# Kernel optimization log

Hardware: AMD Instinct MI355X
Metric: run time of the kernel (lower is better)

Reference implementation:

```python
import jax, jax.numpy as jnp
import numpy as np

N_CLASSES = 18

def setup_inputs() -> dict:
    key = jax.random.key(0)
    k1, k2 = jax.random.split(key)
    B = 2_000_000
    output = jax.random.normal(k1, (B, N_CLASSES), dtype=jnp.float32)
    labels_soft = jax.random.uniform(k2, (B, N_CLASSES), dtype=jnp.float32)
    return {"output": output, "labels_soft": labels_soft}

def reference(output, labels_soft):
    # Original: sum over classes of mean_b( CE(output, cls) * labels_soft[:, cls] )
    # = mean over batch of sum_c( -log_softmax(output)[b, c] * labels_soft[b, c] )
    logp = jax.nn.log_softmax(output, axis=-1)          # [B, C]
    per_row = -jnp.sum(logp * labels_soft, axis=-1)     # [B]
    return jnp.mean(per_row)
```

## Files before the change

kernel.cpp:

```cpp
#include <hip/hip_runtime.h>

#define NCLS   18
#define TROWS  256
#define TWORDS (TROWS * NCLS)
#define NCHUNK ((TWORDS * 4) / 1024)

#define AS1 __attribute__((address_space(1)))
#define AS3 __attribute__((address_space(3)))

__global__ __launch_bounds__(256) void ce_soft_kernel(
    const float* __restrict__ logits,
    const float* __restrict__ labels,
    float* __restrict__ result,
    int B, float invB)
{
    __shared__ float sX[TWORDS];
    __shared__ float sLse[TROWS];

    const int tid  = threadIdx.x;
    const int lane = tid & 63;
    const int wid  = tid >> 6;

    const int nTiles = B / TROWS;
    float acc = 0.0f;

    for (int tile = blockIdx.x; tile < nTiles; tile += gridDim.x) {
        const float* gx = logits + (size_t)tile * TWORDS;

        for (int c = wid; c < NCHUNK; c += 4) {
            __builtin_amdgcn_global_load_lds(
                (const AS1 void*)(gx + c * 256 + lane * 4),
                (AS3 void*)(sX + c * 256),
                16, 0, 0);
        }
        __syncthreads();

        {
            const float2* r2 = (const float2*)(sX + tid * NCLS);
            float x[NCLS];
            #pragma unroll
            for (int k = 0; k < NCLS / 2; ++k) {
                float2 v = r2[k];
                x[2 * k] = v.x; x[2 * k + 1] = v.y;
            }
            float m = x[0];
            #pragma unroll
            for (int c = 1; c < NCLS; ++c) m = fmaxf(m, x[c]);
            float se = 0.0f;
            #pragma unroll
            for (int c = 0; c < NCLS; ++c) se += __expf(x[c] - m);
            sLse[tid] = m + __logf(se);
        }
        __syncthreads();

        const float2* gl2 = (const float2*)(labels + (size_t)tile * TWORDS);
        const float2* sx2 = (const float2*)sX;
        #pragma unroll
        for (int it = 0; it < TWORDS / 512; ++it) {
            int j = it * 256 + tid;
            float2 lv = gl2[j];
            float2 xv = sx2[j];
            float lse = sLse[j / 9];
            acc = fmaf(lv.x, lse - xv.x, acc);
            acc = fmaf(lv.y, lse - xv.y, acc);
        }
        __syncthreads();
    }

    for (int row = nTiles * TROWS + blockIdx.x * blockDim.x + tid; row < B;
         row += gridDim.x * blockDim.x) {
        const float2* o2 = (const float2*)(logits + (size_t)row * NCLS);
        const float2* l2 = (const float2*)(labels + (size_t)row * NCLS);
        float x[NCLS], l[NCLS];
        #pragma unroll
        for (int k = 0; k < NCLS / 2; ++k) {
            float2 v = o2[k]; x[2 * k] = v.x; x[2 * k + 1] = v.y;
            float2 w = l2[k]; l[2 * k] = w.x; l[2 * k + 1] = w.y;
        }
        float m = x[0];
        #pragma unroll
        for (int c = 1; c < NCLS; ++c) m = fmaxf(m, x[c]);
        float se = 0.0f, dot = 0.0f, sl = 0.0f;
        #pragma unroll
        for (int c = 0; c < NCLS; ++c) {
            se += __expf(x[c] - m);
            dot = fmaf(l[c], x[c], dot);
            sl += l[c];
        }
        float lse = m + __logf(se);
        acc = fmaf(sl, lse, acc - dot);
    }

    #pragma unroll
    for (int off = 32; off > 0; off >>= 1)
        acc += __shfl_down(acc, off, 64);

    __shared__ float wave_sums[4];
    if (lane == 0) wave_sums[wid] = acc;
    __syncthreads();
    if (tid == 0) {
        float s = wave_sums[0] + wave_sums[1] + wave_sums[2] + wave_sums[3];
        atomicAdd(result, s * invB);
    }
}

extern "C" void kernel_launch(void* const* d_in, const int* in_sizes, int n_in,
                              void* d_out, int out_size, void* d_ws, size_t ws_size,
                              hipStream_t stream) {
    const float* logits = (const float*)d_in[0];
    const float* labels = (const float*)d_in[1];
    float* result = (float*)d_out;

    int B = in_sizes[0] / NCLS;

    hipMemsetAsync(d_out, 0, sizeof(float), stream);

    int block = 256;
    int grid  = 2048;
    ce_soft_kernel<<<grid, block, 0, stream>>>(logits, labels, result, B, 1.0f / (float)B);
}
```

Measured before the change: 294.9 us.

## Double-buffer logits and labels into LDS and split each row across two threads

Logits and labels tiles now both stream into LDS through async global-to-LDS loads, into double buffers, so the next tile is fetched while the current one is computed. Each row is handled by a pair of threads that combine max and sum-exp with lane shuffles. The tile shrinks to 128 rows and the grid to 1024 blocks. The atomic accumulation and memset are replaced by per-block partials plus a single-block finish kernel. This adds a second launch and relies on the workspace size, and the prefetch loop issues no explicit wait on the async loads before the barrier.

```diff
diff --git a/kernel.cpp b/kernel.cpp
--- a/kernel.cpp
+++ b/kernel.cpp
@@ -1,74 +1,93 @@
 #include <hip/hip_runtime.h>
 
 #define NCLS   18
-#define TROWS  256
+#define TROWS  128
 #define TWORDS (TROWS * NCLS)
-#define NCHUNK ((TWORDS * 4) / 1024)
+#define CHUNKS (TWORDS / 256)
 
 #define AS1 __attribute__((address_space(1)))
 #define AS3 __attribute__((address_space(3)))
 
-__global__ __launch_bounds__(256) void ce_soft_kernel(
+__global__ __launch_bounds__(256) void ce_soft_main(
     const float* __restrict__ logits,
     const float* __restrict__ labels,
-    float* __restrict__ result,
-    int B, float invB)
+    float* __restrict__ partial,
+    int B)
 {
-    __shared__ float sX[TWORDS];
-    __shared__ float sLse[TROWS];
+    __shared__ float sX[2][TWORDS];
+    __shared__ float sL[2][TWORDS];
+    __shared__ float sWS[4];
 
     const int tid  = threadIdx.x;
     const int lane = tid & 63;
     const int wid  = tid >> 6;
+    const int p    = tid >> 1;
+    const int h    = tid & 1;
+    const int nTiles = B / TROWS;
+    const int grid = gridDim.x;
 
-    const int nTiles = B / TROWS;
     float acc = 0.0f;
+    int cur = 0;
 
-    for (int tile = blockIdx.x; tile < nTiles; tile += gridDim.x) {
-        const float* gx = logits + (size_t)tile * TWORDS;
+    int t0 = blockIdx.x;
+    if (t0 < nTiles) {
+        const float* gx = logits + (size_t)t0 * TWORDS;
+        const float* gl = labels + (size_t)t0 * TWORDS;
+        for (int c = wid; c < CHUNKS; c += 4) {
+            __builtin_amdgcn_global_load_lds((const AS1 void*)(gx + c * 256 + lane * 4),
+                                             (AS3 void*)(&sX[0][c * 256]), 16, 0, 0);
+            __builtin_amdgcn_global_load_lds((const AS1 void*)(gl + c * 256 + lane * 4),
+                                             (AS3 void*)(&sL[0][c * 256]), 16, 0, 0);
+        }
+    }
 
-        for (int c = wid; c < NCHUNK; c += 4) {
-            __builtin_amdgcn_global_load_lds(
-                (const AS1 void*)(gx + c * 256 + lane * 4),
-                (AS3 void*)(sX + c * 256),
-                16, 0, 0);
-        }
+    for (int t = t0; t < nTiles; t += grid) {
         __syncthreads();
 
-        {
-            const float2* r2 = (const float2*)(sX + tid * NCLS);
-            float x[NCLS];
-            #pragma unroll
-            for (int k = 0; k < NCLS / 2; ++k) {
-                float2 v = r2[k];
-                x[2 * k] = v.x; x[2 * k + 1] = v.y;
+        int tn = t + grid;
+        if (tn < nTiles) {
+            const float* gx = logits + (size_t)tn * TWORDS;
+            const float* gl = labels + (size_t)tn * TWORDS;
+            float* dX = &sX[cur ^ 1][0];
+            float* dL = &sL[cur ^ 1][0];
+            for (int c = wid; c < CHUNKS; c += 4) {
+                __builtin_amdgcn_global_load_lds((const AS1 void*)(gx + c * 256 + lane * 4),
+                                                 (AS3 void*)(dX + c * 256), 16, 0, 0);
+                __builtin_amdgcn_global_load_lds((const AS1 void*)(gl + c * 256 + lane * 4),
+                                                 (AS3 void*)(dL + c * 256), 16, 0, 0);
             }
-            float m = x[0];
-            #pragma unroll
-            for (int c = 1; c < NCLS; ++c) m = fmaxf(m, x[c]);
-            float se = 0.0f;
-            #pragma unroll
-            for (int c = 0; c < NCLS; ++c) se += __expf(x[c] - m);
-            sLse[tid] = m + __logf(se);
         }
-        __syncthreads();
 
-        const float2* gl2 = (const float2*)(labels + (size_t)tile * TWORDS);
-        const float2* sx2 = (const float2*)sX;
+        const float2* rx = (const float2*)(&sX[cur][p * NCLS]);
+        const float2* rl = (const float2*)(&sL[cur][p * NCLS]);
+        float2 xv[5], lv[5];
+        const int n = 5 - h;
         #pragma unroll
-        for (int it = 0; it < TWORDS / 512; ++it) {
-            int j = it * 256 + tid;
-            float2 lv = gl2[j];
-            float2 xv = sx2[j];
-            float lse = sLse[j / 9];
-            acc = fmaf(lv.x, lse - xv.x, acc);
-            acc = fmaf(lv.y, lse - xv.y, acc);
+        for (int k = 0; k < 5; ++k) {
+            int c = 2 * k + h;
+            if (k < n) { xv[k] = rx[c];                      lv[k] = rl[c]; }
+            else       { xv[k] = make_float2(-1e30f, -1e30f); lv[k] = make_float2(0.f, 0.f); }
         }
-        __syncthreads();
+        float m = xv[0].x;
+        #pragma unroll
+        for (int k = 0; k < 5; ++k) { m = fmaxf(m, xv[k].x); m = fmaxf(m, xv[k].y); }
+        m = fmaxf(m, __shfl_xor(m, 1, 64));
+        float se = 0.f, dot = 0.f, sl = 0.f;
+        #pragma unroll
+        for (int k = 0; k < 5; ++k) {
+            se += __expf(xv[k].x - m) + __expf(xv[k].y - m);
+            dot = fmaf(lv[k].x, xv[k].x, dot);
+            dot = fmaf(lv[k].y, xv[k].y, dot);
+            sl += lv[k].x + lv[k].y;
+        }
+        se += __shfl_xor(se, 1, 64);
+        float lse = m + __logf(se);
+        acc = fmaf(sl, lse, acc - dot);
+        cur ^= 1;
     }
 
     for (int row = nTiles * TROWS + blockIdx.x * blockDim.x + tid; row < B;
-         row += gridDim.x * blockDim.x) {
+         row += grid * blockDim.x) {
         const float2* o2 = (const float2*)(logits + (size_t)row * NCLS);
         const float2* l2 = (const float2*)(labels + (size_t)row * NCLS);
         float x[NCLS], l[NCLS];
@@ -77,31 +96,43 @@
             float2 v = o2[k]; x[2 * k] = v.x; x[2 * k + 1] = v.y;
             float2 w = l2[k]; l[2 * k] = w.x; l[2 * k + 1] = w.y;
         }
-        float m = x[0];
+        float mm = x[0];
         #pragma unroll
-        for (int c = 1; c < NCLS; ++c) m = fmaxf(m, x[c]);
-        float se = 0.0f, dot = 0.0f, sl = 0.0f;
+        for (int c = 1; c < NCLS; ++c) mm = fmaxf(mm, x[c]);
+        float se = 0.f, dot = 0.f, sl = 0.f;
         #pragma unroll
         for (int c = 0; c < NCLS; ++c) {
-            se += __expf(x[c] - m);
+            se += __expf(x[c] - mm);
             dot = fmaf(l[c], x[c], dot);
             sl += l[c];
         }
-        float lse = m + __logf(se);
-        acc = fmaf(sl, lse, acc - dot);
+        acc = fmaf(sl, mm + __logf(se), acc - dot);
     }
 
     #pragma unroll
     for (int off = 32; off > 0; off >>= 1)
         acc += __shfl_down(acc, off, 64);
+    if (lane == 0) sWS[wid] = acc;
+    __syncthreads();
+    if (tid == 0)
+        partial[blockIdx.x] = sWS[0] + sWS[1] + sWS[2] + sWS[3];
+}
 
-    __shared__ float wave_sums[4];
-    if (lane == 0) wave_sums[wid] = acc;
+__global__ __launch_bounds__(256) void ce_soft_finish(
+    const float* __restrict__ partial, float* __restrict__ result,
+    int n, float invB)
+{
+    float s = 0.f;
+    for (int i = threadIdx.x; i < n; i += 256) s += partial[i];
+    #pragma unroll
+    for (int off = 32; off > 0; off >>= 1)
+        s += __shfl_down(s, off, 64);
+    __shared__ float ws[4];
+    int lane = threadIdx.x & 63, wid = threadIdx.x >> 6;
+    if (lane == 0) ws[wid] = s;
     __syncthreads();
-    if (tid == 0) {
-        float s = wave_sums[0] + wave_sums[1] + wave_sums[2] + wave_sums[3];
-        atomicAdd(result, s * invB);
-    }
+    if (threadIdx.x == 0)
+        result[0] = (ws[0] + ws[1] + ws[2] + ws[3]) * invB;
 }
 
 extern "C" void kernel_launch(void* const* d_in, const int* in_sizes, int n_in,
@@ -113,9 +144,15 @@
 
     int B = in_sizes[0] / NCLS;
 
-    hipMemsetAsync(d_out, 0, sizeof(float), stream);
+    int grid = 1024;
+    size_t need = (size_t)grid * sizeof(float);
+    if (ws_size < need) {
+        grid = (int)(ws_size / sizeof(float));
+        if (grid > 1024) grid = 1024;
+        if (grid < 1) grid = 1;
+    }
+    float* partial = (float*)d_ws;
 
-    int block = 256;
-    int grid  = 2048;
-    ce_soft_kernel<<<grid, block, 0, stream>>>(logits, labels, result, B, 1.0f / (float)B);
+    ce_soft_main<<<grid, 256, 0, stream>>>(logits, labels, partial, B);
+    ce_soft_finish<<<1, 256, 0, stream>>>(partial, result, grid, 1.0f / (float)B);
 }
```

Result: faster. 286.7 us (-2.8%).
